# Optimization experiments

Hardware: AMD Instinct MI355X
Metric: run time of the kernel (lower is better)

## Reference

```python
import jax, jax.numpy as jnp
import numpy as np

HEADS = 4
DIM_HEAD = 64
MAP_SIZE = 16
SCALE = DIM_HEAD ** (-0.5)


def _split_heads(x):
    # torch rearrange 'b (dim_head heads) h w -> b heads (h w) dim_head'
    B, C, H, W = x.shape
    x = x.reshape(B, DIM_HEAD, HEADS, H * W)
    return jnp.transpose(x, (0, 2, 3, 1))  # [B, heads, N, dim_head]


def _merge_heads(x, H, W):
    # torch rearrange 'b heads (h w) dim_head -> b (dim_head heads) h w'
    B, h, N, d = x.shape
    return jnp.transpose(x, (0, 3, 1, 2)).reshape(B, d * h, H, W)


def setup_inputs() -> dict:
    key = jax.random.key(0)
    ks = jax.random.split(key, 6)
    feat = jax.random.normal(ks[0], (4, 256, 96, 96), jnp.float32)
    semantic_map = jax.random.normal(ks[1], (4, 256, 16, 16), jnp.float32)
    # 1x1 conv weights, shape [out_ch, in_ch]; scaled like fan-in init
    W_feat_qv = 0.05 * jax.random.normal(ks[2], (512, 256), jnp.float32)
    W_map_qv = 0.05 * jax.random.normal(ks[3], (512, 256), jnp.float32)
    W_feat_out = 0.05 * jax.random.normal(ks[4], (256, 256), jnp.float32)
    W_map_out = 0.05 * jax.random.normal(ks[5], (256, 256), jnp.float32)
    return {
        "feat": feat,
        "semantic_map": semantic_map,
        "W_feat_qv": W_feat_qv,
        "W_map_qv": W_map_qv,
        "W_feat_out": W_feat_out,
        "W_map_out": W_map_out,
    }


def reference(feat, semantic_map, W_feat_qv, W_map_qv, W_feat_out, W_map_out):
    B, C, H, W = feat.shape
    # 1x1 convs == per-pixel channel matmuls
    fqv = jnp.einsum("oc,bchw->bohw", W_feat_qv, feat)
    feat_q, feat_v = jnp.split(fqv, 2, axis=1)
    mqv = jnp.einsum("oc,bchw->bohw", W_map_qv, semantic_map)
    map_q, map_v = jnp.split(mqv, 2, axis=1)

    feat_q, feat_v = _split_heads(feat_q), _split_heads(feat_v)  # [B,h,N,d]
    map_q, map_v = _split_heads(map_q), _split_heads(map_v)      # [B,h,M,d]

    attn = jnp.einsum("bhid,bhjd->bhij", feat_q, map_q) * SCALE  # [B,h,N,M]
    feat_map_attn = jax.nn.softmax(attn, axis=-1)  # normalize over map tokens j
    map_feat_attn = jax.nn.softmax(attn, axis=-2)  # normalize over feat tokens i

    feat_o = jnp.einsum("bhij,bhjd->bhid", feat_map_attn, map_v)   # [B,h,N,d]
    map_o = jnp.einsum("bhji,bhjd->bhid", map_feat_attn, feat_v)   # [B,h,M,d]

    feat_o = _merge_heads(feat_o, H, W)
    map_o = _merge_heads(map_o, MAP_SIZE, MAP_SIZE)

    feat_out = jnp.einsum("oc,bchw->bohw", W_feat_out, feat_o)
    map_out = jnp.einsum("oc,bchw->bohw", W_map_out, map_o)
    return feat_out, map_out
```

## Files before the change

kernel.cpp:

```cpp
#include <hip/hip_runtime.h>
#include <stdint.h>

#define DI static __device__ __forceinline__

constexpr int NTOK = 9216;
constexpr float ATT_SCALE = 0.125f;

typedef short bf16x8 __attribute__((ext_vector_type(8)));
typedef float f32x4  __attribute__((ext_vector_type(4)));

DI f32x4 mfma16(bf16x8 a, bf16x8 b, f32x4 c) {
  return __builtin_amdgcn_mfma_f32_16x16x32_bf16(a, b, c, 0, 0, 0);
}

DI float lo2f(uint32_t u) { union { uint32_t i; float f; } v; v.i = u << 16; return v.f; }
DI float hi2f(uint32_t u) { union { uint32_t i; float f; } v; v.i = u & 0xffff0000u; return v.f; }
DI float b2f(uint16_t u) { union { uint32_t i; float f; } v; v.i = ((uint32_t)u) << 16; return v.f; }
DI uint16_t f2b(float f) {
  union { float f; uint32_t i; } v; v.f = f;
  uint32_t r = (v.i + 0x7fffu + ((v.i >> 16) & 1u)) >> 16;
  return (uint16_t)r;
}

template<int DT> DI float ld1(const void* p, size_t off) {
  if constexpr (DT) return b2f(((const uint16_t*)p)[off]);
  else              return ((const float*)p)[off];
}
template<int DT> DI void st1(void* p, size_t off, float v) {
  if constexpr (DT) ((uint16_t*)p)[off] = f2b(v);
  else              ((float*)p)[off] = v;
}
template<int DT> DI void load8(const void* p, size_t off, float* o) {
  if constexpr (DT) {
    const uint4 w = *(const uint4*)((const uint16_t*)p + off);
    o[0] = lo2f(w.x); o[1] = hi2f(w.x); o[2] = lo2f(w.y); o[3] = hi2f(w.y);
    o[4] = lo2f(w.z); o[5] = hi2f(w.z); o[6] = lo2f(w.w); o[7] = hi2f(w.w);
  } else {
    const float4 a = *(const float4*)((const float*)p + off);
    const float4 b = *(const float4*)((const float*)p + off + 4);
    o[0] = a.x; o[1] = a.y; o[2] = a.z; o[3] = a.w;
    o[4] = b.x; o[5] = b.y; o[6] = b.z; o[7] = b.w;
  }
}

__global__ void detect_dtype(const uint32_t* __restrict__ w, int* __restrict__ flag) {
  if (threadIdx.x == 0 && blockIdx.x == 0) {
    int cl = 0;
    for (int i = 0; i < 256; ++i) {
      const float b = b2f((uint16_t)(w[i] & 0xffffu));
      const float ab = fabsf(b);
      if (ab > 1e-4f && ab < 0.5f) cl++;
    }
    flag[0] = (cl >= 128) ? 1 : 0;
  }
}

template<int DT>
__global__ __launch_bounds__(256) void prep_w(
    const void* __restrict__ Wfqv, const void* __restrict__ Wfo,
    uint16_t* __restrict__ WqvP, uint16_t* __restrict__ WfoP,
    const int* __restrict__ flag)
{
  if (flag[0] != DT) return;
  const int r = blockIdx.x, c = threadIdx.x;
  if (r < 512) {
    const int sel = r >> 8, within = r & 255;
    const int h = within >> 6, d = within & 63;
    const int src = sel * 256 + d * 4 + h;
    const int q = (c >> 3) & 3, j = c & 7;
    const int kp = (c & ~31) | (q << 3) | ((j + 2 * q) & 7);
    WqvP[(size_t)r * 256 + c] = f2b(ld1<DT>(Wfqv, (size_t)src * 256 + kp));
  } else {
    const int ro = r - 512;
    WfoP[(size_t)ro * 256 + c] =
        f2b(ld1<DT>(Wfo, (size_t)ro * 256 + (c & 63) * 4 + (c >> 6)));
  }
}

constexpr int PB = 264;

template<int DT>
__global__ __launch_bounds__(256) void gemm0_mfma(
    const uint16_t* __restrict__ WqvP, const void* __restrict__ X,
    uint16_t* __restrict__ FQ, uint16_t* __restrict__ FV,
    const int* __restrict__ flag)
{
  if (flag[0] != DT) return;
  __shared__ __align__(16) uint16_t Bsh[32 * PB];
  const int tid = threadIdx.x;
  const int w = tid >> 6, lane = tid & 63;
  const int l = lane & 15, quad = lane >> 4;
  const int n0 = blockIdx.x * 256;
  const int hh = blockIdx.y;
  const int bb = blockIdx.z;
  const size_t bh = (size_t)bb * 4 + hh;

  f32x4 acc[8][4];
  #pragma unroll
  for (int a = 0; a < 8; ++a)
    #pragma unroll
    for (int b = 0; b < 4; ++b) { acc[a][b].x = 0.f; acc[a][b].y = 0.f; acc[a][b].z = 0.f; acc[a][b].w = 0.f; }

  const int cst = tid >> 3;
  const int nst = (tid & 7) * 32;

  for (int ks = 0; ks < 8; ++ks) {
    {
      const size_t gbase = ((size_t)bb * 256 + ks * 32 + cst) * NTOK + n0 + nst;
      #pragma unroll
      for (int q = 0; q < 4; ++q) {
        if constexpr (DT) {
          *(uint4*)(Bsh + cst * PB + nst + q * 8) =
              *(const uint4*)((const uint16_t*)X + gbase + q * 8);
        } else {
          float xv[8];
          load8<0>(X, gbase + q * 8, xv);
          uint16_t pk[8];
          #pragma unroll
          for (int j = 0; j < 8; ++j) pk[j] = f2b(xv[j]);
          *(uint4*)(Bsh + cst * PB + nst + q * 8) = *(const uint4*)pk;
        }
      }
    }
    __syncthreads();
    bf16x8 af[8];
    #pragma unroll
    for (int mt = 0; mt < 8; ++mt) {
      const int arow = (mt >> 2) * 256 + hh * 64 + (mt & 3) * 16 + l;
      af[mt] = *(const bf16x8*)(WqvP + (size_t)arow * 256 + ks * 32 + quad * 8);
    }
    #pragma unroll
    for (int nt = 0; nt < 4; ++nt) {
      const int nl = w * 64 + nt * 16 + l;
      union { uint16_t h[8]; bf16x8 v; } bu;
      #pragma unroll
      for (int j = 0; j < 8; ++j)
        bu.h[j] = Bsh[(quad * 8 + ((j + 2 * quad) & 7)) * PB + nl];
      #pragma unroll
      for (int mt = 0; mt < 8; ++mt)
        acc[mt][nt] = mfma16(af[mt], bu.v, acc[mt][nt]);
    }
    __syncthreads();
  }
  #pragma unroll
  for (int mt = 0; mt < 8; ++mt)
    #pragma unroll
    for (int nt = 0; nt < 4; ++nt) {
      const int n = n0 + w * 64 + nt * 16 + l;
      if (mt < 4) {
        union { uint16_t h[4]; uint2 u; } pk;
        #pragma unroll
        for (int r = 0; r < 4; ++r) pk.h[r] = f2b(acc[mt][nt][r]);
        *(uint2*)(FQ + (bh * NTOK + n) * 64 + mt * 16 + quad * 4) = pk.u;
      } else {
        #pragma unroll
        for (int r = 0; r < 4; ++r)
          FV[(bh * 64 + (mt - 4) * 16 + quad * 4 + r) * NTOK + n] =
              f2b(acc[mt][nt][r]);
      }
    }
}

template<int DT>
__global__ __launch_bounds__(256) void gemm1_mfma(
    const uint16_t* __restrict__ WfoP, const uint16_t* __restrict__ FO,
    void* __restrict__ out, const int* __restrict__ flag)
{
  if (flag[0] != DT) return;
  const int tid = threadIdx.x;
  const int w = tid >> 6, lane = tid & 63;
  const int l = lane & 15, quad = lane >> 4;
  const int n0 = blockIdx.x * 256;
  const int o0 = blockIdx.y * 64;
  const int bb = blockIdx.z;

  f32x4 acc[4][4];
  #pragma unroll
  for (int a = 0; a < 4; ++a)
    #pragma unroll
    for (int b = 0; b < 4; ++b) { acc[a][b].x = 0.f; acc[a][b].y = 0.f; acc[a][b].z = 0.f; acc[a][b].w = 0.f; }

  for (int ks = 0; ks < 8; ++ks) {
    const int h2 = ks >> 1;
    const int doff = (ks & 1) * 32 + quad * 8;
    bf16x8 af[4];
    #pragma unroll
    for (int mt = 0; mt < 4; ++mt)
      af[mt] = *(const bf16x8*)(WfoP + (size_t)(o0 + mt * 16 + l) * 256 + ks * 32 + quad * 8);
    #pragma unroll
    for (int nt = 0; nt < 4; ++nt) {
      const int n = n0 + w * 64 + nt * 16 + l;
      const bf16x8 bv = *(const bf16x8*)(FO + ((size_t)(bb * 4 + h2) * NTOK + n) * 64 + doff);
      #pragma unroll
      for (int mt = 0; mt < 4; ++mt)
        acc[mt][nt] = mfma16(af[mt], bv, acc[mt][nt]);
    }
  }
  #pragma unroll
  for (int mt = 0; mt < 4; ++mt)
    #pragma unroll
    for (int nt = 0; nt < 4; ++nt) {
      const int n = n0 + w * 64 + nt * 16 + l;
      #pragma unroll
      for (int r = 0; r < 4; ++r)
        st1<DT>(out, ((size_t)bb * 256 + o0 + mt * 16 + quad * 4 + r) * NTOK + n,
                acc[mt][nt][r]);
    }
}

template<int DT>
__global__ __launch_bounds__(256) void map_qv(
    const void* __restrict__ Wqv, const void* __restrict__ smap,
    uint16_t* __restrict__ MQ, uint16_t* __restrict__ MVT,
    const int* __restrict__ flag)
{
  if (flag[0] != DT) return;
  const int o = blockIdx.x, bb = blockIdx.y, m = threadIdx.x;
  float acc = 0.f;
  #pragma unroll 8
  for (int c = 0; c < 256; ++c)
    acc += ld1<DT>(Wqv, (size_t)o * 256 + c) *
           ld1<DT>(smap, (size_t)bb * 65536 + (size_t)c * 256 + m);
  const int oc = o & 255;
  const int h = oc & 3, d = oc >> 2;
  if (o < 256) MQ[(((size_t)bb * 4 + h) * 256 + m) * 64 + d] = f2b(acc);
  else         MVT[(((size_t)bb * 4 + h) * 64 + d) * 256 + m] = f2b(acc);
}

constexpr int PJ = 264;
constexpr int PI = 48;

__global__ __launch_bounds__(256, 3) void attn_mfma(
    const uint16_t* __restrict__ FQ, const uint16_t* __restrict__ FV,
    const uint16_t* __restrict__ MQ, const uint16_t* __restrict__ MVT,
    uint16_t* __restrict__ FO, float* __restrict__ NUM, float* __restrict__ CS)
{
  __shared__ __align__(16) uint16_t Esh[32 * PJ];
  __shared__ __align__(16) uint16_t ETsh[256 * PI];
  __shared__ float RS[4][32];
  const int tid = threadIdx.x;
  const int w = tid >> 6;
  const int lane = tid & 63;
  const int l = lane & 15, quad = lane >> 4;
  const int blk = blockIdx.x, bh = blockIdx.y;
  const uint16_t* FQh  = FQ  + (size_t)bh * NTOK * 64;
  const uint16_t* FVh  = FV  + (size_t)bh * 64 * NTOK;
  const uint16_t* MQh  = MQ  + (size_t)bh * 256 * 64;
  const uint16_t* MVTh = MVT + (size_t)bh * 64 * 256;
  uint16_t* FOh = FO + (size_t)bh * NTOK * 64;

  f32x4 numacc[4][4];
  #pragma unroll
  for (int a = 0; a < 4; ++a)
    #pragma unroll
    for (int b = 0; b < 4; ++b) { numacc[a][b].x = 0.f; numacc[a][b].y = 0.f; numacc[a][b].z = 0.f; numacc[a][b].w = 0.f; }
  float csum[4] = {0.f, 0.f, 0.f, 0.f};

  for (int t = 0; t < 6; ++t) {
    const int i0 = (blk * 6 + t) * 32;

    bf16x8 qa[2][2];
    #pragma unroll
    for (int mt = 0; mt < 2; ++mt)
      #pragma unroll
      for (int kb = 0; kb < 2; ++kb)
        qa[mt][kb] = *(const bf16x8*)(FQh + (size_t)(i0 + mt * 16 + l) * 64 + kb * 32 + quad * 8);
    float rsum[2][4] = {{0.f,0.f,0.f,0.f},{0.f,0.f,0.f,0.f}};
    #pragma unroll
    for (int jt = 0; jt < 4; ++jt) {
      const int j0 = w * 64 + jt * 16;
      const bf16x8 kb0 = *(const bf16x8*)(MQh + (size_t)(j0 + l) * 64 + quad * 8);
      const bf16x8 kb1 = *(const bf16x8*)(MQh + (size_t)(j0 + l) * 64 + 32 + quad * 8);
      #pragma unroll
      for (int mt = 0; mt < 2; ++mt) {
        f32x4 acc = {0.f, 0.f, 0.f, 0.f};
        acc = mfma16(qa[mt][0], kb0, acc);
        acc = mfma16(qa[mt][1], kb1, acc);
        union { uint16_t h[4]; uint2 u; } pk;
        #pragma unroll
        for (int r = 0; r < 4; ++r) {
          const float e = __expf(acc[r] * ATT_SCALE);
          rsum[mt][r] += e;
          csum[jt] += e;
          pk.h[r] = f2b(e);
          Esh[(mt * 16 + quad * 4 + r) * PJ + j0 + l] = pk.h[r];
        }
        *(uint2*)(ETsh + (size_t)(j0 + l) * PI + mt * 16 + quad * 4) = pk.u;
      }
    }
    #pragma unroll
    for (int mt = 0; mt < 2; ++mt)
      #pragma unroll
      for (int r = 0; r < 4; ++r) {
        float v = rsum[mt][r];
        v += __shfl_xor(v, 1); v += __shfl_xor(v, 2);
        v += __shfl_xor(v, 4); v += __shfl_xor(v, 8);
        if (l == 0) RS[w][mt * 16 + quad * 4 + r] = v;
      }
    __syncthreads();

    {
      float rinv[2];
      #pragma unroll
      for (int nt = 0; nt < 2; ++nt) {
        const int i_ = nt * 16 + l;
        rinv[nt] = 1.f / (RS[0][i_] + RS[1][i_] + RS[2][i_] + RS[3][i_]);
      }
      f32x4 oacc[2];
      oacc[0].x=0.f;oacc[0].y=0.f;oacc[0].z=0.f;oacc[0].w=0.f;
      oacc[1]=oacc[0];
      #pragma unroll
      for (int ks = 0; ks < 8; ++ks) {
        const bf16x8 av = *(const bf16x8*)(MVTh + (size_t)(w * 16 + l) * 256 + ks * 32 + quad * 8);
        #pragma unroll
        for (int nt = 0; nt < 2; ++nt) {
          const bf16x8 bv = *(const bf16x8*)(Esh + (size_t)(nt * 16 + l) * PJ + ks * 32 + quad * 8);
          oacc[nt] = mfma16(av, bv, oacc[nt]);
        }
      }
      #pragma unroll
      for (int nt = 0; nt < 2; ++nt) {
        union { uint16_t h[4]; uint2 u; } pk;
        #pragma unroll
        for (int r = 0; r < 4; ++r) pk.h[r] = f2b(oacc[nt][r] * rinv[nt]);
        *(uint2*)(FOh + (size_t)(i0 + nt * 16 + l) * 64 + w * 16 + quad * 4) = pk.u;
      }
    }

    #pragma unroll
    for (int mt = 0; mt < 4; ++mt) {
      const bf16x8 av = *(const bf16x8*)(FVh + (size_t)(mt * 16 + l) * NTOK + i0 + quad * 8);
      #pragma unroll
      for (int nt2 = 0; nt2 < 4; ++nt2) {
        const bf16x8 bv = *(const bf16x8*)(ETsh + (size_t)(w * 64 + nt2 * 16 + l) * PI + quad * 8);
        numacc[mt][nt2] = mfma16(av, bv, numacc[mt][nt2]);
      }
    }
    __syncthreads();
  }

  #pragma unroll
  for (int jt = 0; jt < 4; ++jt) {
    float v = csum[jt];
    v += __shfl_xor(v, 16); v += __shfl_xor(v, 32);
    if (quad == 0) atomicAdd(&CS[(size_t)bh * 256 + w * 64 + jt * 16 + l], v);
  }
  #pragma unroll
  for (int mt = 0; mt < 4; ++mt)
    #pragma unroll
    for (int nt2 = 0; nt2 < 4; ++nt2)
      #pragma unroll
      for (int r = 0; r < 4; ++r)
        atomicAdd(&NUM[((size_t)bh * 64 + mt * 16 + quad * 4 + r) * 256 + w * 64 + nt2 * 16 + l],
                  numacc[mt][nt2][r]);
}

__global__ __launch_bounds__(256) void final_div(
    const float* __restrict__ NUM, const float* __restrict__ CS,
    uint16_t* __restrict__ MO)
{
  const int idx = blockIdx.x * 256 + threadIdx.x;
  const int bh = idx >> 14;
  const int d = (idx >> 8) & 63;
  const int j = idx & 255;
  const float v = NUM[idx] / CS[(bh << 8) + j];
  const int b = bh >> 2, h = bh & 3;
  MO[((size_t)b * 256 + (d * 4 + h)) * 256 + j] = f2b(v);
}

template<int DT>
__global__ __launch_bounds__(256) void map_out_k(
    const void* __restrict__ Wmo, const uint16_t* __restrict__ MO,
    void* __restrict__ out, const int* __restrict__ flag)
{
  if (flag[0] != DT) return;
  const int o = blockIdx.x, bb = blockIdx.y, m = threadIdx.x;
  float acc = 0.f;
  #pragma unroll 8
  for (int c = 0; c < 256; ++c)
    acc += ld1<DT>(Wmo, (size_t)o * 256 + c) *
           b2f(MO[((size_t)bb * 256 + c) * 256 + m]);
  const size_t MAP_OFS = (size_t)4 * 256 * NTOK;
  st1<DT>(out, MAP_OFS + ((size_t)bb * 256 + o) * 256 + m, acc);
}

extern "C" void kernel_launch(void* const* d_in, const int* in_sizes, int n_in,
                              void* d_out, int out_size, void* d_ws, size_t ws_size,
                              hipStream_t stream) {
  (void)in_sizes; (void)n_in; (void)out_size; (void)ws_size;
  const void* feat = d_in[0];
  const void* smap = d_in[1];
  const void* Wfqv = d_in[2];
  const void* Wmqv = d_in[3];
  const void* Wfo  = d_in[4];
  const void* Wmo  = d_in[5];
  char* ws = (char*)d_ws;

  const size_t BIG = (size_t)16 * 64 * NTOK * 2;
  const size_t SML = (size_t)16 * 256 * 64 * 2;
  const size_t FQ_OFF  = 0;
  const size_t FV_OFF  = FQ_OFF + BIG;
  const size_t MQ_OFF  = FV_OFF + BIG;
  const size_t MVT_OFF = MQ_OFF + SML;
  const size_t MO_OFF  = MVT_OFF + SML;
  const size_t NUM_OFF = MO_OFF + (size_t)4 * 256 * 256 * 2;
  const size_t NUM_BYTES = (size_t)16 * 64 * 256 * 4;
  const size_t CS_BYTES  = (size_t)16 * 256 * 4;
  const size_t WQP_OFF   = NUM_OFF + NUM_BYTES + CS_BYTES;
  const size_t WFP_OFF   = WQP_OFF + (size_t)512 * 256 * 2;
  const size_t FLAG_OFF  = WFP_OFF + (size_t)256 * 256 * 2;

  uint16_t* FQ   = (uint16_t*)(ws + FQ_OFF);
  uint16_t* FV   = (uint16_t*)(ws + FV_OFF);
  uint16_t* MQ   = (uint16_t*)(ws + MQ_OFF);
  uint16_t* MVT  = (uint16_t*)(ws + MVT_OFF);
  uint16_t* MO   = (uint16_t*)(ws + MO_OFF);
  float* NUM  = (float*)(ws + NUM_OFF);
  float* CS   = (float*)(ws + NUM_OFF + NUM_BYTES);
  uint16_t* WqvP = (uint16_t*)(ws + WQP_OFF);
  uint16_t* WfoP = (uint16_t*)(ws + WFP_OFF);
  int* FLAG   = (int*)(ws + FLAG_OFF);

  detect_dtype<<<dim3(1), dim3(64), 0, stream>>>((const uint32_t*)Wfqv, FLAG);
  hipMemsetAsync(ws + NUM_OFF, 0, NUM_BYTES + CS_BYTES, stream);

  prep_w<0><<<dim3(768), 256, 0, stream>>>(Wfqv, Wfo, WqvP, WfoP, FLAG);
  prep_w<1><<<dim3(768), 256, 0, stream>>>(Wfqv, Wfo, WqvP, WfoP, FLAG);
  gemm0_mfma<0><<<dim3(36, 4, 4), 256, 0, stream>>>(WqvP, feat, FQ, FV, FLAG);
  gemm0_mfma<1><<<dim3(36, 4, 4), 256, 0, stream>>>(WqvP, feat, FQ, FV, FLAG);
  map_qv<0><<<dim3(512, 4), 256, 0, stream>>>(Wmqv, smap, MQ, MVT, FLAG);
  map_qv<1><<<dim3(512, 4), 256, 0, stream>>>(Wmqv, smap, MQ, MVT, FLAG);
  attn_mfma<<<dim3(48, 16), 256, 0, stream>>>(FQ, FV, MQ, MVT, FQ, NUM, CS);
  gemm1_mfma<0><<<dim3(36, 4, 4), 256, 0, stream>>>(WfoP, FQ, d_out, FLAG);
  gemm1_mfma<1><<<dim3(36, 4, 4), 256, 0, stream>>>(WfoP, FQ, d_out, FLAG);
  final_div<<<dim3(1024), 256, 0, stream>>>(NUM, CS, MO);
  map_out_k<0><<<dim3(256, 4), 256, 0, stream>>>(Wmo, MO, d_out, FLAG);
  map_out_k<1><<<dim3(256, 4), 256, 0, stream>>>(Wmo, MO, d_out, FLAG);
}
```

Measured before the change: 350.6 us.

## Replace atomic map-numerator accumulation with bf16 partials reduced in a separate kernel

The attention kernel now writes per-block partial numerators and column sums as bf16 into a scratch area (the output buffer, before gemm1 overwrites it) instead of issuing fp32 atomicAdds. The grid shrinks from 48 to 32 blocks per head, with each block covering 9 tiles, so there are fewer partials to store. A new reduce_map kernel sums the partials and divides, replacing final_div, and the memset is dropped. This removes atomic contention and the memset, but the partial sums are rounded to bf16 before reduction, which lowers accuracy, and the smaller grid lowers parallelism.

```diff
diff --git a/kernel.cpp b/kernel.cpp
--- a/kernel.cpp
+++ b/kernel.cpp
@@ -229,11 +229,12 @@
 
 constexpr int PJ = 264;
 constexpr int PI = 48;
+constexpr int NGRP = 32;
 
 __global__ __launch_bounds__(256, 3) void attn_mfma(
     const uint16_t* __restrict__ FQ, const uint16_t* __restrict__ FV,
     const uint16_t* __restrict__ MQ, const uint16_t* __restrict__ MVT,
-    uint16_t* __restrict__ FO, float* __restrict__ NUM, float* __restrict__ CS)
+    uint16_t* __restrict__ FO, uint16_t* __restrict__ P)
 {
   __shared__ __align__(16) uint16_t Esh[32 * PJ];
   __shared__ __align__(16) uint16_t ETsh[256 * PI];
@@ -256,8 +257,8 @@
     for (int b = 0; b < 4; ++b) { numacc[a][b].x = 0.f; numacc[a][b].y = 0.f; numacc[a][b].z = 0.f; numacc[a][b].w = 0.f; }
   float csum[4] = {0.f, 0.f, 0.f, 0.f};
 
-  for (int t = 0; t < 6; ++t) {
-    const int i0 = (blk * 6 + t) * 32;
+  for (int t = 0; t < 9; ++t) {
+    const int i0 = (blk * 9 + t) * 32;
 
     bf16x8 qa[2][2];
     #pragma unroll
@@ -339,31 +340,38 @@
     __syncthreads();
   }
 
+  uint16_t* Pb = P + ((size_t)bh * NGRP + blk) * 65 * 256;
+  #pragma unroll
+  for (int mt = 0; mt < 4; ++mt)
+    #pragma unroll
+    for (int nt2 = 0; nt2 < 4; ++nt2)
+      #pragma unroll
+      for (int r = 0; r < 4; ++r)
+        Pb[(mt * 16 + quad * 4 + r) * 256 + w * 64 + nt2 * 16 + l] =
+            f2b(numacc[mt][nt2][r]);
   #pragma unroll
   for (int jt = 0; jt < 4; ++jt) {
     float v = csum[jt];
     v += __shfl_xor(v, 16); v += __shfl_xor(v, 32);
-    if (quad == 0) atomicAdd(&CS[(size_t)bh * 256 + w * 64 + jt * 16 + l], v);
-  }
-  #pragma unroll
-  for (int mt = 0; mt < 4; ++mt)
-    #pragma unroll
-    for (int nt2 = 0; nt2 < 4; ++nt2)
-      #pragma unroll
-      for (int r = 0; r < 4; ++r)
-        atomicAdd(&NUM[((size_t)bh * 64 + mt * 16 + quad * 4 + r) * 256 + w * 64 + nt2 * 16 + l],
-                  numacc[mt][nt2][r]);
-}
-
-__global__ __launch_bounds__(256) void final_div(
-    const float* __restrict__ NUM, const float* __restrict__ CS,
-    uint16_t* __restrict__ MO)
+    if (quad == 0) Pb[64 * 256 + w * 64 + jt * 16 + l] = f2b(v);
+  }
+}
+
+__global__ __launch_bounds__(256) void reduce_map(
+    const uint16_t* __restrict__ P, uint16_t* __restrict__ MO)
 {
   const int idx = blockIdx.x * 256 + threadIdx.x;
   const int bh = idx >> 14;
   const int d = (idx >> 8) & 63;
   const int j = idx & 255;
-  const float v = NUM[idx] / CS[(bh << 8) + j];
+  const size_t base = (size_t)bh * NGRP * 65 * 256;
+  float num = 0.f, cs = 0.f;
+  #pragma unroll 8
+  for (int g = 0; g < NGRP; ++g) {
+    num += b2f(P[base + ((size_t)g * 65 + d) * 256 + j]);
+    cs  += b2f(P[base + ((size_t)g * 65 + 64) * 256 + j]);
+  }
+  const float v = num / cs;
   const int b = bh >> 2, h = bh & 3;
   MO[((size_t)b * 256 + (d * 4 + h)) * 256 + j] = f2b(v);
 }
@@ -403,26 +411,22 @@
   const size_t MQ_OFF  = FV_OFF + BIG;
   const size_t MVT_OFF = MQ_OFF + SML;
   const size_t MO_OFF  = MVT_OFF + SML;
-  const size_t NUM_OFF = MO_OFF + (size_t)4 * 256 * 256 * 2;
-  const size_t NUM_BYTES = (size_t)16 * 64 * 256 * 4;
-  const size_t CS_BYTES  = (size_t)16 * 256 * 4;
-  const size_t WQP_OFF   = NUM_OFF + NUM_BYTES + CS_BYTES;
-  const size_t WFP_OFF   = WQP_OFF + (size_t)512 * 256 * 2;
-  const size_t FLAG_OFF  = WFP_OFF + (size_t)256 * 256 * 2;
+  const size_t WQP_OFF = MO_OFF + (size_t)4 * 256 * 256 * 2;
+  const size_t WFP_OFF = WQP_OFF + (size_t)512 * 256 * 2;
+  const size_t FLAG_OFF = WFP_OFF + (size_t)256 * 256 * 2;
 
   uint16_t* FQ   = (uint16_t*)(ws + FQ_OFF);
   uint16_t* FV   = (uint16_t*)(ws + FV_OFF);
   uint16_t* MQ   = (uint16_t*)(ws + MQ_OFF);
   uint16_t* MVT  = (uint16_t*)(ws + MVT_OFF);
   uint16_t* MO   = (uint16_t*)(ws + MO_OFF);
-  float* NUM  = (float*)(ws + NUM_OFF);
-  float* CS   = (float*)(ws + NUM_OFF + NUM_BYTES);
   uint16_t* WqvP = (uint16_t*)(ws + WQP_OFF);
   uint16_t* WfoP = (uint16_t*)(ws + WFP_OFF);
   int* FLAG   = (int*)(ws + FLAG_OFF);
 
+  uint16_t* P = (uint16_t*)d_out;
+
   detect_dtype<<<dim3(1), dim3(64), 0, stream>>>((const uint32_t*)Wfqv, FLAG);
-  hipMemsetAsync(ws + NUM_OFF, 0, NUM_BYTES + CS_BYTES, stream);
 
   prep_w<0><<<dim3(768), 256, 0, stream>>>(Wfqv, Wfo, WqvP, WfoP, FLAG);
   prep_w<1><<<dim3(768), 256, 0, stream>>>(Wfqv, Wfo, WqvP, WfoP, FLAG);
@@ -430,10 +434,10 @@
   gemm0_mfma<1><<<dim3(36, 4, 4), 256, 0, stream>>>(WqvP, feat, FQ, FV, FLAG);
   map_qv<0><<<dim3(512, 4), 256, 0, stream>>>(Wmqv, smap, MQ, MVT, FLAG);
   map_qv<1><<<dim3(512, 4), 256, 0, stream>>>(Wmqv, smap, MQ, MVT, FLAG);
-  attn_mfma<<<dim3(48, 16), 256, 0, stream>>>(FQ, FV, MQ, MVT, FQ, NUM, CS);
+  attn_mfma<<<dim3(NGRP, 16), 256, 0, stream>>>(FQ, FV, MQ, MVT, FQ, P);
+  reduce_map<<<dim3(1024), 256, 0, stream>>>(P, MO);
   gemm1_mfma<0><<<dim3(36, 4, 4), 256, 0, stream>>>(WfoP, FQ, d_out, FLAG);
   gemm1_mfma<1><<<dim3(36, 4, 4), 256, 0, stream>>>(WfoP, FQ, d_out, FLAG);
-  final_div<<<dim3(1024), 256, 0, stream>>>(NUM, CS, MO);
   map_out_k<0><<<dim3(256, 4), 256, 0, stream>>>(Wmo, MO, d_out, FLAG);
   map_out_k<1><<<dim3(256, 4), 256, 0, stream>>>(Wmo, MO, d_out, FLAG);
 }
```

Measured after the change: 337.8 us. 1.04x faster.
